# Optimization experiments

Hardware: AMD Instinct MI355X
Metric: run time of the kernel (lower is better)

Reference implementation:

```python
import jax, jax.numpy as jnp
import numpy as np

N_NODES = 50000
N_EDGES = 800000
D = 64
N_GRAPHS = 512
N_LAYERS = 3
HID_FC = 64
N_CLASSES = 10


def setup_inputs() -> dict:
    key = jax.random.key(0)
    ks = jax.random.split(key, 12)
    s = 1.0 / np.sqrt(D)
    x = jax.random.normal(ks[0], (N_NODES, D), dtype=jnp.float32)
    edge_index = jax.random.randint(ks[1], (2, N_EDGES), 0, N_NODES, dtype=jnp.int32)
    batch = jnp.sort(jax.random.randint(ks[2], (N_NODES,), 0, N_GRAPHS, dtype=jnp.int32))
    convW1 = jax.random.normal(ks[3], (N_LAYERS, D, D), dtype=jnp.float32) * s
    convb1 = jax.random.normal(ks[4], (N_LAYERS, D), dtype=jnp.float32) * 0.01
    convW2 = jax.random.normal(ks[5], (N_LAYERS, D, D), dtype=jnp.float32) * s
    convb2 = jax.random.normal(ks[6], (N_LAYERS, D), dtype=jnp.float32) * 0.01
    fcW1 = jax.random.normal(ks[7], (D, HID_FC), dtype=jnp.float32) * s
    fcb1 = jax.random.normal(ks[8], (HID_FC,), dtype=jnp.float32) * 0.01
    fcW2 = jax.random.normal(ks[9], (HID_FC, N_CLASSES), dtype=jnp.float32) * (1.0 / np.sqrt(HID_FC))
    fcb2 = jax.random.normal(ks[10], (N_CLASSES,), dtype=jnp.float32) * 0.01
    return {"x": x, "convW1": convW1, "convb1": convb1, "convW2": convW2,
            "convb2": convb2, "fcW1": fcW1, "fcb1": fcb1, "fcW2": fcW2,
            "fcb2": fcb2, "edge_index": edge_index, "batch": batch}


def reference(x, convW1, convb1, convW2, convb2, fcW1, fcb1, fcW2, fcb2, edge_index, batch):
    src, dst = edge_index[0], edge_index[1]
    h = x
    for l in range(N_LAYERS):
        # GIN aggregation: (1 + eps) * x + sum_{j in N(i)} x_j, eps = 0
        agg = jax.ops.segment_sum(h[src], dst, num_segments=N_NODES)
        h = h + agg
        # per-layer MLP: Linear -> ReLU -> Linear
        h = jax.nn.relu(h @ convW1[l] + convb1[l])
        h = h @ convW2[l] + convb2[l]
    # global max pool over nodes of each graph
    g = jax.ops.segment_max(h, batch, num_segments=N_GRAPHS)
    # FC head: Linear(64) -> ReLU -> Linear(num_classes)
    g = jax.nn.relu(g @ fcW1 + fcb1)
    logits = g @ fcW2 + fcb2
    return jax.nn.log_softmax(logits, axis=1)
```

## Files before the change

### kernel.cpp

```cpp
#include <hip/hip_runtime.h>
#include <math.h>

#define N_NODES 50000
#define N_EDGES 800000
#define D 64
#define N_GRAPHS 512
#define N_CLASSES 10
#define NT 3125

#define SCAN_B 512
#define NB_SCAN ((N_NODES + SCAN_B - 1) / SCAN_B)

typedef __attribute__((ext_vector_type(8))) short bf16x8;
typedef __attribute__((ext_vector_type(4))) float f32x4;

#define MFMA16(a, b, c) __builtin_amdgcn_mfma_f32_16x16x32_bf16(a, b, c, 0, 0, 0)


__device__ __forceinline__ unsigned mapf(float f) {
  unsigned u = __float_as_uint(f);
  return (u & 0x80000000u) ? ~u : (u | 0x80000000u);
}
__device__ __forceinline__ float unmapf(unsigned u) {
  return __uint_as_float((u & 0x80000000u) ? (u & 0x7FFFFFFFu) : ~u);
}
__device__ __forceinline__ ushort bf16_rne(float f) {
  unsigned u = __float_as_uint(f);
  u += 0x7FFFu + ((u >> 16) & 1u);
  return (ushort)(u >> 16);
}
__device__ __forceinline__ float bf16_tof(ushort h) {
  return __uint_as_float(((unsigned)h) << 16);
}


__global__ void wprep(const float* __restrict__ convW1, const float* __restrict__ convW2,
                      ushort* __restrict__ wf) {
  const int wi = blockIdx.x;
  const int layer = wi >> 1, which = wi & 1;
  const float* W = (which ? convW2 : convW1) + layer * 4096;
  const int t = threadIdx.x;
  const int f = t >> 6, lane = t & 63;
  const int ct = f >> 1, ks = f & 1;
  const int n = ct * 16 + (lane & 15);
  const int k0 = ks * 32 + ((lane >> 4) << 3);
  ushort hi[8], lo[8];
#pragma unroll
  for (int v = 0; v < 8; ++v) {
    float w = W[(k0 + v) * 64 + n];
    ushort h = bf16_rne(w);
    hi[v] = h;
    lo[v] = bf16_rne(w - bf16_tof(h));
  }
  *(uint4*)(wf + ((wi * 2 + 0) * 8 + f) * 512 + lane * 8) = *(uint4*)hi;
  *(uint4*)(wf + ((wi * 2 + 1) * 8 + f) * 512 + lane * 8) = *(uint4*)lo;
}


__global__ void hist_kernel(const int* __restrict__ dst, int* __restrict__ deg) {
  int e = blockIdx.x * 256 + threadIdx.x;
  if (e < N_EDGES) atomicAdd(&deg[dst[e]], 1);
}

__global__ void scan_blocks(const int* __restrict__ deg, int* __restrict__ bsum) {
  __shared__ int sd[SCAN_B];
  int i = blockIdx.x * SCAN_B + threadIdx.x;
  sd[threadIdx.x] = (i < N_NODES) ? deg[i] : 0;
  __syncthreads();
  for (int off = SCAN_B / 2; off > 0; off >>= 1) {
    if (threadIdx.x < off) sd[threadIdx.x] += sd[threadIdx.x + off];
    __syncthreads();
  }
  if (threadIdx.x == 0) bsum[blockIdx.x] = sd[0];
}

__global__ void scan_mid(int* __restrict__ bsum) {
  __shared__ int s[256];
  int t = threadIdx.x;
  if (t < NB_SCAN) s[t] = bsum[t];
  __syncthreads();
  if (t == 0) {
    int run = 0;
    for (int i = 0; i < NB_SCAN; ++i) { int v = s[i]; s[i] = run; run += v; }
  }
  __syncthreads();
  if (t < NB_SCAN) bsum[t] = s[t];
}

__global__ void scan_final(const int* __restrict__ deg, const int* __restrict__ bsum,
                           int* __restrict__ rs, int* __restrict__ cur) {
  __shared__ int sd[SCAN_B];
  int i = blockIdx.x * SCAN_B + threadIdx.x;
  int v = (i < N_NODES) ? deg[i] : 0;
  sd[threadIdx.x] = v;
  __syncthreads();
  for (int off = 1; off < SCAN_B; off <<= 1) {
    int add = (threadIdx.x >= off) ? sd[threadIdx.x - off] : 0;
    __syncthreads();
    sd[threadIdx.x] += add;
    __syncthreads();
  }
  if (i < N_NODES) {
    int ex = bsum[blockIdx.x] + sd[threadIdx.x] - v;
    rs[i] = ex;
    cur[i] = ex;
  }
  if (i == 0) rs[N_NODES] = N_EDGES;
}

__global__ void fill_csr(const int* __restrict__ src, const int* __restrict__ dst,
                         int* __restrict__ cur, int* __restrict__ csr) {
  int e = blockIdx.x * 256 + threadIdx.x;
  if (e >= N_EDGES) return;
  int p = atomicAdd(&cur[dst[e]], 1);
  csr[p] = src[e];
}


__global__ __launch_bounds__(256) void agg_f32(
    const float* __restrict__ hin, const int* __restrict__ csr,
    const int* __restrict__ rs, float* __restrict__ acc) {
  const int t = threadIdx.x;
  const int hw = t >> 5, hl = t & 31;
  const int node = blockIdx.x * 8 + hw;
  const float2* __restrict__ H = (const float2*)hin;
  float2 a = H[node * 32 + hl];
  int e = rs[node];
  const int e1 = rs[node + 1];
  for (; e + 4 <= e1; e += 4) {
    int s0 = csr[e], s1 = csr[e + 1], s2 = csr[e + 2], s3 = csr[e + 3];
    float2 v0 = H[s0 * 32 + hl];
    float2 v1 = H[s1 * 32 + hl];
    float2 v2 = H[s2 * 32 + hl];
    float2 v3 = H[s3 * 32 + hl];
    a.x += v0.x + v1.x; a.y += v0.y + v1.y;
    a.x += v2.x + v3.x; a.y += v2.y + v3.y;
  }
  for (; e < e1; ++e) {
    float2 v = H[csr[e] * 32 + hl];
    a.x += v.x; a.y += v.y;
  }
  ((float2*)acc)[node * 32 + hl] = a;
}


template <int FINAL>
__global__ __launch_bounds__(256) void mlp_mfma(
    float* __restrict__ A,
    const ushort* __restrict__ wfL,
    const float* __restrict__ b1, const float* __restrict__ b2,
    const int* __restrict__ batch, unsigned* __restrict__ gU) {
  __shared__ char ldsraw[4][5504];
  const int t = threadIdx.x;
  const int w = t >> 6, lane = t & 63;
  const int tile = blockIdx.x * 4 + w;
  if (tile >= NT) return;
  const int m = lane & 15, g = lane >> 4;
  char* lds = ldsraw[w];

  const float* Ar = A + (size_t)(tile * 16 + m) * 64;
  bf16x8 aH[2], aL[2];
#pragma unroll
  for (int ks = 0; ks < 2; ++ks) {
    float4 f0 = ((const float4*)Ar)[(ks * 32 + g * 8) >> 2];
    float4 f1 = ((const float4*)Ar)[((ks * 32 + g * 8) >> 2) + 1];
    float v[8] = {f0.x, f0.y, f0.z, f0.w, f1.x, f1.y, f1.z, f1.w};
#pragma unroll
    for (int e = 0; e < 8; ++e) {
      ushort h = bf16_rne(v[e]);
      aH[ks][e] = (short)h;
      aL[ks][e] = (short)bf16_rne(v[e] - bf16_tof(h));
    }
  }

  bf16x8 w1h[8], w1l[8];
#pragma unroll
  for (int f = 0; f < 8; ++f) {
    w1h[f] = *(const bf16x8*)(wfL + f * 512 + lane * 8);
    w1l[f] = *(const bf16x8*)(wfL + 4096 + f * 512 + lane * 8);
  }

  f32x4 acc1[4];
#pragma unroll
  for (int ct = 0; ct < 4; ++ct) {
    f32x4 c = {0.f, 0.f, 0.f, 0.f};
    c = MFMA16(aH[0], w1h[ct * 2 + 0], c);
    c = MFMA16(aH[1], w1h[ct * 2 + 1], c);
    c = MFMA16(aL[0], w1h[ct * 2 + 0], c);
    c = MFMA16(aL[1], w1h[ct * 2 + 1], c);
    c = MFMA16(aH[0], w1l[ct * 2 + 0], c);
    c = MFMA16(aH[1], w1l[ct * 2 + 1], c);
    acc1[ct] = c;
  }

  ushort* Hhi = (ushort*)lds;
  ushort* Hlo = (ushort*)(lds + 2560);
#pragma unroll
  for (int ct = 0; ct < 4; ++ct) {
    float bias = b1[ct * 16 + m];
#pragma unroll
    for (int j = 0; j < 4; ++j) {
      float hv = fmaxf(acc1[ct][j] + bias, 0.f);
      ushort hh = bf16_rne(hv);
      int idx = (g * 4 + j) * 80 + ct * 16 + m;
      Hhi[idx] = hh;
      Hlo[idx] = bf16_rne(hv - bf16_tof(hh));
    }
  }

  bf16x8 hH[2], hL[2];
#pragma unroll
  for (int ks = 0; ks < 2; ++ks) {
    hH[ks] = *(const bf16x8*)(Hhi + m * 80 + ks * 32 + g * 8);
    hL[ks] = *(const bf16x8*)(Hlo + m * 80 + ks * 32 + g * 8);
  }

  bf16x8 w2h[8], w2l[8];
#pragma unroll
  for (int f = 0; f < 8; ++f) {
    w2h[f] = *(const bf16x8*)(wfL + 8192 + f * 512 + lane * 8);
    w2l[f] = *(const bf16x8*)(wfL + 12288 + f * 512 + lane * 8);
  }
  f32x4 acc2[4];
#pragma unroll
  for (int ct = 0; ct < 4; ++ct) {
    f32x4 c = {0.f, 0.f, 0.f, 0.f};
    c = MFMA16(hH[0], w2h[ct * 2 + 0], c);
    c = MFMA16(hH[1], w2h[ct * 2 + 1], c);
    c = MFMA16(hL[0], w2h[ct * 2 + 0], c);
    c = MFMA16(hL[1], w2h[ct * 2 + 1], c);
    c = MFMA16(hH[0], w2l[ct * 2 + 0], c);
    c = MFMA16(hH[1], w2l[ct * 2 + 1], c);
    acc2[ct] = c;
  }

  if (FINAL) {
    int b4[4];
#pragma unroll
    for (int j = 0; j < 4; ++j) b4[j] = batch[tile * 16 + g * 4 + j];
#pragma unroll
    for (int ct = 0; ct < 4; ++ct) {
      float bias = b2[ct * 16 + m];
#pragma unroll
      for (int j = 0; j < 4; ++j) {
        float v = acc2[ct][j] + bias;
        atomicMax(&gU[b4[j] * 64 + ct * 16 + m], mapf(v));
      }
    }
  } else {
    float* O = (float*)lds;
#pragma unroll
    for (int ct = 0; ct < 4; ++ct) {
      float bias = b2[ct * 16 + m];
#pragma unroll
      for (int j = 0; j < 4; ++j)
        O[(g * 4 + j) * 84 + ct * 16 + m] = acc2[ct][j] + bias;
    }
    float* Aw = A + (size_t)(tile * 16 + m) * 64;
#pragma unroll
    for (int q = 0; q < 4; ++q) {
      float4 vv = *(const float4*)(O + m * 84 + g * 16 + q * 4);
      ((float4*)Aw)[g * 4 + q] = vv;
    }
  }
}


__global__ void init_g(unsigned* __restrict__ gU) {
  int i = blockIdx.x * blockDim.x + threadIdx.x;
  if (i < N_GRAPHS * D) gU[i] = 0x007FFFFFu;
}

__global__ void head_kernel(const unsigned* __restrict__ gU,
                            const float* __restrict__ fcW1, const float* __restrict__ fcb1,
                            const float* __restrict__ fcW2, const float* __restrict__ fcb2,
                            float* __restrict__ out) {
  __shared__ float gbuf[64];
  __shared__ float hid[64];
  __shared__ float logit[N_CLASSES];
  __shared__ float red[2];
  const int gi = blockIdx.x;
  const int t = threadIdx.x;

  gbuf[t] = unmapf(gU[gi * D + t]);
  __syncthreads();

  float a = fcb1[t];
#pragma unroll
  for (int k = 0; k < 64; ++k) a = fmaf(gbuf[k], fcW1[k * 64 + t], a);
  hid[t] = fmaxf(a, 0.0f);
  __syncthreads();

  if (t < N_CLASSES) {
    float l = fcb2[t];
#pragma unroll
    for (int k = 0; k < 64; ++k) l = fmaf(hid[k], fcW2[k * N_CLASSES + t], l);
    logit[t] = l;
  }
  __syncthreads();

  if (t == 0) {
    float mx = logit[0];
    for (int i = 1; i < N_CLASSES; ++i) mx = fmaxf(mx, logit[i]);
    float s = 0.0f;
    for (int i = 0; i < N_CLASSES; ++i) s += expf(logit[i] - mx);
    red[0] = mx;
    red[1] = logf(s);
  }
  __syncthreads();

  if (t < N_CLASSES) out[gi * N_CLASSES + t] = logit[t] - red[0] - red[1];
}


extern "C" void kernel_launch(void* const* d_in, const int* in_sizes, int n_in,
                              void* d_out, int out_size, void* d_ws, size_t ws_size,
                              hipStream_t stream) {
  const float* x      = (const float*)d_in[0];
  const float* convW1 = (const float*)d_in[1];
  const float* convb1 = (const float*)d_in[2];
  const float* convW2 = (const float*)d_in[3];
  const float* convb2 = (const float*)d_in[4];
  const float* fcW1   = (const float*)d_in[5];
  const float* fcb1   = (const float*)d_in[6];
  const float* fcW2   = (const float*)d_in[7];
  const float* fcb2   = (const float*)d_in[8];
  const int*   edge   = (const int*)d_in[9];
  const int*   batch  = (const int*)d_in[10];
  float* out = (float*)d_out;

  const int* src = edge;
  const int* dst = edge + N_EDGES;

  float* accA = (float*)d_ws;
  float* accB = accA + (size_t)N_NODES * 64;
  unsigned* gU = (unsigned*)(accB + (size_t)N_NODES * 64);
  int* rs  = (int*)(gU + N_GRAPHS * D);
  int* csr = rs + N_NODES + 1;
  ushort* wf = (ushort*)(csr + N_EDGES);
  int* deg  = (int*)accA;
  int* cur  = deg + N_NODES;
  int* bsum = cur + N_NODES;

  wprep<<<6, 512, 0, stream>>>(convW1, convW2, wf);
  init_g<<<(N_GRAPHS * D + 255) / 256, 256, 0, stream>>>(gU);

  hipMemsetAsync(deg, 0, N_NODES * sizeof(int), stream);
  hist_kernel<<<N_EDGES / 256, 256, 0, stream>>>(dst, deg);
  scan_blocks<<<NB_SCAN, SCAN_B, 0, stream>>>(deg, bsum);
  scan_mid<<<1, 256, 0, stream>>>(bsum);
  scan_final<<<NB_SCAN, SCAN_B, 0, stream>>>(deg, bsum, rs, cur);
  fill_csr<<<N_EDGES / 256, 256, 0, stream>>>(src, dst, cur, csr);

  const int AGG_B = N_NODES / 8;
  const int MLP_B = (NT + 3) / 4;
  agg_f32<<<AGG_B, 256, 0, stream>>>(x, csr, rs, accA);
  mlp_mfma<0><<<MLP_B, 256, 0, stream>>>(accA, wf, convb1, convb2, batch, gU);
  agg_f32<<<AGG_B, 256, 0, stream>>>(accA, csr, rs, accB);
  mlp_mfma<0><<<MLP_B, 256, 0, stream>>>(accB, wf + 16384, convb1 + 64, convb2 + 64,
                                         batch, gU);
  agg_f32<<<AGG_B, 256, 0, stream>>>(accB, csr, rs, accA);
  mlp_mfma<1><<<MLP_B, 256, 0, stream>>>(accA, wf + 32768, convb1 + 128, convb2 + 128,
                                         batch, gU);

  head_kernel<<<N_GRAPHS, 64, 0, stream>>>(gU, fcW1, fcb1, fcW2, fcb2, out);
}
```

Baseline: 278.0 us.

## Stage MLP weights in shared LDS and cut per-wave register and LDS use

Each block now copies the layer's bf16 hi/lo weight fragments (32 KB) into LDS once. The MFMAs then read weights from LDS instead of each wave holding 32 fragment registers loaded from global memory. The hidden hi/lo tiles reuse a single per-wave 2560-byte buffer in two passes. The output LDS transpose is dropped in favour of direct strided scalar stores to global memory. This targets register pressure and redundant global weight loads, at the cost of a block-wide sync, a large LDS footprint that may limit occupancy, and less coalesced output writes.

```diff
diff --git a/kernel.cpp b/kernel.cpp
--- a/kernel.cpp
+++ b/kernel.cpp
@@ -31,6 +31,18 @@
 }
 __device__ __forceinline__ float bf16_tof(ushort h) {
   return __uint_as_float(((unsigned)h) << 16);
+}
+
+__device__ __forceinline__ void split8(float4 p0, float4 p1, bf16x8& H, bf16x8& L) {
+  ushort h;
+  h = bf16_rne(p0.x); H[0] = (short)h; L[0] = (short)bf16_rne(p0.x - bf16_tof(h));
+  h = bf16_rne(p0.y); H[1] = (short)h; L[1] = (short)bf16_rne(p0.y - bf16_tof(h));
+  h = bf16_rne(p0.z); H[2] = (short)h; L[2] = (short)bf16_rne(p0.z - bf16_tof(h));
+  h = bf16_rne(p0.w); H[3] = (short)h; L[3] = (short)bf16_rne(p0.w - bf16_tof(h));
+  h = bf16_rne(p1.x); H[4] = (short)h; L[4] = (short)bf16_rne(p1.x - bf16_tof(h));
+  h = bf16_rne(p1.y); H[5] = (short)h; L[5] = (short)bf16_rne(p1.y - bf16_tof(h));
+  h = bf16_rne(p1.z); H[6] = (short)h; L[6] = (short)bf16_rne(p1.z - bf16_tof(h));
+  h = bf16_rne(p1.w); H[7] = (short)h; L[7] = (short)bf16_rne(p1.w - bf16_tof(h));
 }
 
 
@@ -52,8 +64,9 @@
     hi[v] = h;
     lo[v] = bf16_rne(w - bf16_tof(h));
   }
-  *(uint4*)(wf + ((wi * 2 + 0) * 8 + f) * 512 + lane * 8) = *(uint4*)hi;
-  *(uint4*)(wf + ((wi * 2 + 1) * 8 + f) * 512 + lane * 8) = *(uint4*)lo;
+  ushort* base = wf + layer * 16384 + which * 8192;
+  *(uint4*)(base + f * 512 + lane * 8) = *(uint4*)hi;
+  *(uint4*)(base + 4096 + f * 512 + lane * 8) = *(uint4*)lo;
 }
 
 
@@ -150,118 +163,118 @@
     const ushort* __restrict__ wfL,
     const float* __restrict__ b1, const float* __restrict__ b2,
     const int* __restrict__ batch, unsigned* __restrict__ gU) {
-  __shared__ char ldsraw[4][5504];
+  __shared__ char lds[32768 + 4 * 2560];
   const int t = threadIdx.x;
   const int w = t >> 6, lane = t & 63;
+
+  {
+    const uint4* s = (const uint4*)wfL;
+    uint4* d = (uint4*)lds;
+#pragma unroll
+    for (int i = 0; i < 8; ++i) d[t + 256 * i] = s[t + 256 * i];
+  }
+  __syncthreads();
+
   const int tile = blockIdx.x * 4 + w;
   if (tile >= NT) return;
   const int m = lane & 15, g = lane >> 4;
-  char* lds = ldsraw[w];
+  const char* wb = lds + lane * 16;
+  ushort* tb16 = (ushort*)(lds + 32768 + w * 2560);
 
   const float* Ar = A + (size_t)(tile * 16 + m) * 64;
-  bf16x8 aH[2], aL[2];
-#pragma unroll
-  for (int ks = 0; ks < 2; ++ks) {
-    float4 f0 = ((const float4*)Ar)[(ks * 32 + g * 8) >> 2];
-    float4 f1 = ((const float4*)Ar)[((ks * 32 + g * 8) >> 2) + 1];
-    float v[8] = {f0.x, f0.y, f0.z, f0.w, f1.x, f1.y, f1.z, f1.w};
-#pragma unroll
-    for (int e = 0; e < 8; ++e) {
-      ushort h = bf16_rne(v[e]);
-      aH[ks][e] = (short)h;
-      aL[ks][e] = (short)bf16_rne(v[e] - bf16_tof(h));
-    }
-  }
-
-  bf16x8 w1h[8], w1l[8];
-#pragma unroll
-  for (int f = 0; f < 8; ++f) {
-    w1h[f] = *(const bf16x8*)(wfL + f * 512 + lane * 8);
-    w1l[f] = *(const bf16x8*)(wfL + 4096 + f * 512 + lane * 8);
-  }
-
-  f32x4 acc1[4];
-#pragma unroll
-  for (int ct = 0; ct < 4; ++ct) {
-    f32x4 c = {0.f, 0.f, 0.f, 0.f};
-    c = MFMA16(aH[0], w1h[ct * 2 + 0], c);
-    c = MFMA16(aH[1], w1h[ct * 2 + 1], c);
-    c = MFMA16(aL[0], w1h[ct * 2 + 0], c);
-    c = MFMA16(aL[1], w1h[ct * 2 + 1], c);
-    c = MFMA16(aH[0], w1l[ct * 2 + 0], c);
-    c = MFMA16(aH[1], w1l[ct * 2 + 1], c);
-    acc1[ct] = c;
-  }
-
-  ushort* Hhi = (ushort*)lds;
-  ushort* Hlo = (ushort*)(lds + 2560);
-#pragma unroll
-  for (int ct = 0; ct < 4; ++ct) {
-    float bias = b1[ct * 16 + m];
-#pragma unroll
-    for (int j = 0; j < 4; ++j) {
-      float hv = fmaxf(acc1[ct][j] + bias, 0.f);
-      ushort hh = bf16_rne(hv);
-      int idx = (g * 4 + j) * 80 + ct * 16 + m;
-      Hhi[idx] = hh;
-      Hlo[idx] = bf16_rne(hv - bf16_tof(hh));
-    }
-  }
-
-  bf16x8 hH[2], hL[2];
-#pragma unroll
-  for (int ks = 0; ks < 2; ++ks) {
-    hH[ks] = *(const bf16x8*)(Hhi + m * 80 + ks * 32 + g * 8);
-    hL[ks] = *(const bf16x8*)(Hlo + m * 80 + ks * 32 + g * 8);
-  }
-
-  bf16x8 w2h[8], w2l[8];
-#pragma unroll
-  for (int f = 0; f < 8; ++f) {
-    w2h[f] = *(const bf16x8*)(wfL + 8192 + f * 512 + lane * 8);
-    w2l[f] = *(const bf16x8*)(wfL + 12288 + f * 512 + lane * 8);
-  }
-  f32x4 acc2[4];
-#pragma unroll
-  for (int ct = 0; ct < 4; ++ct) {
-    f32x4 c = {0.f, 0.f, 0.f, 0.f};
-    c = MFMA16(hH[0], w2h[ct * 2 + 0], c);
-    c = MFMA16(hH[1], w2h[ct * 2 + 1], c);
-    c = MFMA16(hL[0], w2h[ct * 2 + 0], c);
-    c = MFMA16(hL[1], w2h[ct * 2 + 1], c);
-    c = MFMA16(hH[0], w2l[ct * 2 + 0], c);
-    c = MFMA16(hH[1], w2l[ct * 2 + 1], c);
-    acc2[ct] = c;
-  }
-
+  bf16x8 aH0, aH1, aL0, aL1;
+  {
+    float4 p0 = *(const float4*)(Ar + g * 8);
+    float4 p1 = *(const float4*)(Ar + g * 8 + 4);
+    float4 p2 = *(const float4*)(Ar + 32 + g * 8);
+    float4 p3 = *(const float4*)(Ar + 32 + g * 8 + 4);
+    split8(p0, p1, aH0, aL0);
+    split8(p2, p3, aH1, aL1);
+  }
+
+#define LDW(off) (*(const bf16x8*)(wb + (off)))
+
+  f32x4 c1_0 = {0.f, 0.f, 0.f, 0.f}, c1_1 = c1_0, c1_2 = c1_0, c1_3 = c1_0;
+#define G1(ct, cc)                                   \
+  cc = MFMA16(aH0, LDW((2 * ct + 0) * 1024), cc);    \
+  cc = MFMA16(aH1, LDW((2 * ct + 1) * 1024), cc);    \
+  cc = MFMA16(aL0, LDW((2 * ct + 0) * 1024), cc);    \
+  cc = MFMA16(aL1, LDW((2 * ct + 1) * 1024), cc);    \
+  cc = MFMA16(aH0, LDW(8192 + (2 * ct + 0) * 1024), cc); \
+  cc = MFMA16(aH1, LDW(8192 + (2 * ct + 1) * 1024), cc);
+  G1(0, c1_0) G1(1, c1_1) G1(2, c1_2) G1(3, c1_3)
+#undef G1
+
+  {
+    float bv0 = b1[m], bv1 = b1[16 + m], bv2 = b1[32 + m], bv3 = b1[48 + m];
+#define BR(cc, bv)                     \
+    cc[0] = fmaxf(cc[0] + bv, 0.f);    \
+    cc[1] = fmaxf(cc[1] + bv, 0.f);    \
+    cc[2] = fmaxf(cc[2] + bv, 0.f);    \
+    cc[3] = fmaxf(cc[3] + bv, 0.f);
+    BR(c1_0, bv0) BR(c1_1, bv1) BR(c1_2, bv2) BR(c1_3, bv3)
+#undef BR
+  }
+
+#define WRH(cc, ct)                                                    \
+  tb16[(g * 4 + 0) * 80 + ct * 16 + m] = bf16_rne(cc[0]);              \
+  tb16[(g * 4 + 1) * 80 + ct * 16 + m] = bf16_rne(cc[1]);              \
+  tb16[(g * 4 + 2) * 80 + ct * 16 + m] = bf16_rne(cc[2]);              \
+  tb16[(g * 4 + 3) * 80 + ct * 16 + m] = bf16_rne(cc[3]);
+  WRH(c1_0, 0) WRH(c1_1, 1) WRH(c1_2, 2) WRH(c1_3, 3)
+#undef WRH
+  bf16x8 hH0 = *(const bf16x8*)(tb16 + m * 80 + g * 8);
+  bf16x8 hH1 = *(const bf16x8*)(tb16 + m * 80 + 32 + g * 8);
+
+#define WRL(cc, ct)                                                                  \
+  { float hv; ushort hh;                                                             \
+    hv = cc[0]; hh = bf16_rne(hv);                                                   \
+    tb16[(g * 4 + 0) * 80 + ct * 16 + m] = bf16_rne(hv - bf16_tof(hh));              \
+    hv = cc[1]; hh = bf16_rne(hv);                                                   \
+    tb16[(g * 4 + 1) * 80 + ct * 16 + m] = bf16_rne(hv - bf16_tof(hh));              \
+    hv = cc[2]; hh = bf16_rne(hv);                                                   \
+    tb16[(g * 4 + 2) * 80 + ct * 16 + m] = bf16_rne(hv - bf16_tof(hh));              \
+    hv = cc[3]; hh = bf16_rne(hv);                                                   \
+    tb16[(g * 4 + 3) * 80 + ct * 16 + m] = bf16_rne(hv - bf16_tof(hh)); }
+  WRL(c1_0, 0) WRL(c1_1, 1) WRL(c1_2, 2) WRL(c1_3, 3)
+#undef WRL
+  bf16x8 hL0 = *(const bf16x8*)(tb16 + m * 80 + g * 8);
+  bf16x8 hL1 = *(const bf16x8*)(tb16 + m * 80 + 32 + g * 8);
+
+  f32x4 c2_0 = {0.f, 0.f, 0.f, 0.f}, c2_1 = c2_0, c2_2 = c2_0, c2_3 = c2_0;
+#define G2(ct, cc)                                          \
+  cc = MFMA16(hH0, LDW(16384 + (2 * ct + 0) * 1024), cc);   \
+  cc = MFMA16(hH1, LDW(16384 + (2 * ct + 1) * 1024), cc);   \
+  cc = MFMA16(hL0, LDW(16384 + (2 * ct + 0) * 1024), cc);   \
+  cc = MFMA16(hL1, LDW(16384 + (2 * ct + 1) * 1024), cc);   \
+  cc = MFMA16(hH0, LDW(24576 + (2 * ct + 0) * 1024), cc);   \
+  cc = MFMA16(hH1, LDW(24576 + (2 * ct + 1) * 1024), cc);
+  G2(0, c2_0) G2(1, c2_1) G2(2, c2_2) G2(3, c2_3)
+#undef G2
+#undef LDW
+
+  float bv0 = b2[m], bv1 = b2[16 + m], bv2 = b2[32 + m], bv3 = b2[48 + m];
   if (FINAL) {
-    int b4[4];
-#pragma unroll
-    for (int j = 0; j < 4; ++j) b4[j] = batch[tile * 16 + g * 4 + j];
-#pragma unroll
-    for (int ct = 0; ct < 4; ++ct) {
-      float bias = b2[ct * 16 + m];
-#pragma unroll
-      for (int j = 0; j < 4; ++j) {
-        float v = acc2[ct][j] + bias;
-        atomicMax(&gU[b4[j] * 64 + ct * 16 + m], mapf(v));
-      }
-    }
+    int b40 = batch[tile * 16 + g * 4 + 0];
+    int b41 = batch[tile * 16 + g * 4 + 1];
+    int b42 = batch[tile * 16 + g * 4 + 2];
+    int b43 = batch[tile * 16 + g * 4 + 3];
+#define PM(cc, ct, bv)                                          \
+    atomicMax(&gU[b40 * 64 + ct * 16 + m], mapf(cc[0] + bv));   \
+    atomicMax(&gU[b41 * 64 + ct * 16 + m], mapf(cc[1] + bv));   \
+    atomicMax(&gU[b42 * 64 + ct * 16 + m], mapf(cc[2] + bv));   \
+    atomicMax(&gU[b43 * 64 + ct * 16 + m], mapf(cc[3] + bv));
+    PM(c2_0, 0, bv0) PM(c2_1, 1, bv1) PM(c2_2, 2, bv2) PM(c2_3, 3, bv3)
+#undef PM
   } else {
-    float* O = (float*)lds;
-#pragma unroll
-    for (int ct = 0; ct < 4; ++ct) {
-      float bias = b2[ct * 16 + m];
-#pragma unroll
-      for (int j = 0; j < 4; ++j)
-        O[(g * 4 + j) * 84 + ct * 16 + m] = acc2[ct][j] + bias;
-    }
-    float* Aw = A + (size_t)(tile * 16 + m) * 64;
-#pragma unroll
-    for (int q = 0; q < 4; ++q) {
-      float4 vv = *(const float4*)(O + m * 84 + g * 16 + q * 4);
-      ((float4*)Aw)[g * 4 + q] = vv;
-    }
+    float* Aw = A + (size_t)tile * 1024;
+#define ST(cc, ct, bv)                                         \
+    Aw[(g * 4 + 0) * 64 + ct * 16 + m] = cc[0] + bv;           \
+    Aw[(g * 4 + 1) * 64 + ct * 16 + m] = cc[1] + bv;           \
+    Aw[(g * 4 + 2) * 64 + ct * 16 + m] = cc[2] + bv;           \
+    Aw[(g * 4 + 3) * 64 + ct * 16 + m] = cc[3] + bv;
+    ST(c2_0, 0, bv0) ST(c2_1, 1, bv1) ST(c2_2, 2, bv2) ST(c2_3, 3, bv3)
+#undef ST
   }
 }
 
```

Measured after the change: 268.0 us. -3.6%, faster.
